# Kernel optimization log

Hardware: AMD Instinct MI355X
Metric: run time of the kernel (lower is better)

## Reference

```python
import jax, jax.numpy as jnp
import numpy as np
from math import pi

BS, H, C = 4096, 1024, 512
H2, C2 = H // 2, C // 2


def _cm(x, y):
    # complex multiply with real/imag stored in last dim
    return jnp.stack([x[..., 0] * y[..., 0] - x[..., 1] * y[..., 1],
                      x[..., 0] * y[..., 1] + x[..., 1] * y[..., 0]], -1)


def _interleave(a, b):
    # (H2, C2),(H2, C2) -> (H, C2) rows [a0,b0,a1,b1,...]
    return jnp.stack([a, b], 1).reshape(-1, a.shape[1])


def _rotations(phi, theta):
    cp, sp = jnp.cos(phi), jnp.sin(phi)
    ct, st = jnp.cos(theta), jnp.sin(theta)
    z = jnp.zeros_like(ct)
    diag = jnp.stack([_interleave(cp * ct, ct), _interleave(sp * ct, z)], -1)      # (H, C2, 2)
    offd = jnp.stack([_interleave(-cp * st, st), _interleave(-sp * st, z)], -1)    # (H, C2, 2)
    return diag.transpose(1, 0, 2), offd.transpose(1, 0, 2)                        # (C2, H, 2)


def _swap_pairs(x):
    # swap elements within adjacent pairs along the hidden axis
    bs, h, _ = x.shape
    return x.reshape(bs, h // 2, 2, 2)[:, :, ::-1, :].reshape(bs, h, 2)


def setup_inputs() -> dict:
    key = jax.random.key(0)
    ks = jax.random.split(key, 5)
    x = jax.random.normal(ks[0], (BS, H, 2), dtype=jnp.float32)
    phi0 = 2 * pi * jax.random.normal(ks[1], (H2, C2), dtype=jnp.float32)
    theta0 = 2 * pi * jax.random.normal(ks[2], (H2, C2), dtype=jnp.float32)
    phi1 = 2 * pi * jax.random.normal(ks[3], (H2, C2), dtype=jnp.float32)
    theta1 = 2 * pi * jax.random.normal(ks[4], (H2, C2), dtype=jnp.float32)
    return {"x": x, "phi0": phi0, "theta0": theta0, "phi1": phi1, "theta1": theta1}


def reference(x, phi0, theta0, phi1, theta1):
    d0, o0 = _rotations(phi0, theta0)
    d1, o1 = _rotations(phi1, theta1)

    def step(xc, dd):
        dd0, oo0, dd1, oo1 = dd
        xc = _cm(xc, dd0) + _cm(_swap_pairs(xc), oo0)
        xc = jnp.roll(xc, -1, axis=1)   # cat(x[1:], x[:1])
        xc = _cm(xc, dd1) + _cm(_swap_pairs(xc), oo1)
        xc = jnp.roll(xc, 1, axis=1)    # cat(x[-1:], x[:-1])
        return xc, None

    x, _ = jax.lax.scan(step, x, (d0, o0, d1, o1))
    return x
```

## Files before the change

### kernel.cpp

```cpp
#include <hip/hip_runtime.h>


#define H_DIM 1024
#define C2 256
#define RPW 2


__global__ __launch_bounds__(256) void eunn_coef_kernel(
    const float* __restrict__ phi0, const float* __restrict__ theta0,
    const float* __restrict__ phi1, const float* __restrict__ theta1,
    float4* __restrict__ coef) {
    int t = blockIdx.x * 256 + threadIdx.x;
    int i = t & 511;
    int p = (t >> 9) & 1;
    int c = t >> 10;
    const float* phi   = p ? phi1   : phi0;
    const float* theta = p ? theta1 : theta0;
    float ph = phi[i * C2 + c];
    float th = theta[i * C2 + c];
    float sp, cp, st, ct;
    __sincosf(ph, &sp, &cp);
    __sincosf(th, &st, &ct);
    int j = i & 7;
    int l = i >> 3;
    coef[(((c * 2 + p) * 8) + j) * 64 + l] = make_float4(ct, st, cp, sp);
}

__device__ __forceinline__ void rot_pair(const float4 q,
                                         float& ur, float& ui,
                                         float& wr, float& wi) {
    float ar = fmaf(-q.y, wr, q.x * ur);
    float ai = fmaf(-q.y, wi, q.x * ui);
    float br = fmaf( q.x, wr, q.y * ur);
    float bi = fmaf( q.x, wi, q.y * ui);
    ur = fmaf(-q.w, ai, q.z * ar);
    ui = fmaf( q.w, ar, q.z * ai);
    wr = br;
    wi = bi;
}

__global__ __launch_bounds__(256, 2) void eunn_main_kernel(
    const float* __restrict__ x,
    const float4* __restrict__ coef,
    float* __restrict__ out) {
    const int lane = threadIdx.x & 63;
    const int wave = threadIdx.x >> 6;
    const int row0 = (blockIdx.x * 4 + wave) * RPW;

    float vr[RPW][16], vi[RPW][16];

#pragma unroll
    for (int r = 0; r < RPW; ++r) {
        const float4* src = (const float4*)(x + (size_t)(row0 + r) * (H_DIM * 2)) + lane * 8;
#pragma unroll
        for (int m = 0; m < 8; ++m) {
            float4 f = src[m];
            vr[r][2 * m]     = f.x; vi[r][2 * m]     = f.y;
            vr[r][2 * m + 1] = f.z; vi[r][2 * m + 1] = f.w;
        }
    }

    const float4* cl = coef + lane;

#pragma unroll 1
    for (int c = 0; c < C2; ++c) {
        const float4* ca = cl + (size_t)c * 1024;

        float4 qq = ca[15 * 64];
        float qpx = __shfl(qq.x, (lane + 63) & 63);
        float qpy = __shfl(qq.y, (lane + 63) & 63);

        {
            float4 q0 = ca[0 * 64];
            float4 q7 = ca[7 * 64];
#pragma unroll
            for (int r = 0; r < RPW; ++r) {
                rot_pair(q0, vr[r][0],  vi[r][0],  vr[r][1],  vi[r][1]);
                rot_pair(q7, vr[r][14], vi[r][14], vr[r][15], vi[r][15]);
            }
        }
        float nbr[RPW], nbi[RPW], pbr[RPW], pbi[RPW];
#pragma unroll
        for (int r = 0; r < RPW; ++r) {
            nbr[r] = __shfl(vr[r][0],  (lane + 1)  & 63);
            nbi[r] = __shfl(vi[r][0],  (lane + 1)  & 63);
            pbr[r] = __shfl(vr[r][15], (lane + 63) & 63);
            pbi[r] = __shfl(vi[r][15], (lane + 63) & 63);
        }

#pragma unroll
        for (int j = 1; j < 7; ++j) {
            float4 q = ca[j * 64];
#pragma unroll
            for (int r = 0; r < RPW; ++r) {
                rot_pair(q, vr[r][2 * j],     vi[r][2 * j],
                            vr[r][2 * j + 1], vi[r][2 * j + 1]);
            }
        }

#pragma unroll
        for (int j = 0; j < 7; ++j) {
            float4 q = ca[(8 + j) * 64];
#pragma unroll
            for (int r = 0; r < RPW; ++r) {
                rot_pair(q, vr[r][2 * j + 1], vi[r][2 * j + 1],
                            vr[r][2 * j + 2], vi[r][2 * j + 2]);
            }
        }

#pragma unroll
        for (int r = 0; r < RPW; ++r) {
            float ar = fmaf(-qq.y, nbr[r], qq.x * vr[r][15]);
            float ai = fmaf(-qq.y, nbi[r], qq.x * vi[r][15]);
            vr[r][15] = fmaf(-qq.w, ai, qq.z * ar);
            vi[r][15] = fmaf( qq.w, ar, qq.z * ai);
            float b0r = fmaf(qpx, vr[r][0], qpy * pbr[r]);
            float b0i = fmaf(qpx, vi[r][0], qpy * pbi[r]);
            vr[r][0] = b0r; vi[r][0] = b0i;
        }
    }

#pragma unroll
    for (int r = 0; r < RPW; ++r) {
        float4* dst = (float4*)(out + (size_t)(row0 + r) * (H_DIM * 2)) + lane * 8;
#pragma unroll
        for (int m = 0; m < 8; ++m) {
            dst[m] = make_float4(vr[r][2 * m],     vi[r][2 * m],
                                 vr[r][2 * m + 1], vi[r][2 * m + 1]);
        }
    }
}

extern "C" void kernel_launch(void* const* d_in, const int* in_sizes, int n_in,
                              void* d_out, int out_size, void* d_ws, size_t ws_size,
                              hipStream_t stream) {
    const float* x      = (const float*)d_in[0];
    const float* phi0   = (const float*)d_in[1];
    const float* theta0 = (const float*)d_in[2];
    const float* phi1   = (const float*)d_in[3];
    const float* theta1 = (const float*)d_in[4];
    float* out = (float*)d_out;
    float4* coef = (float4*)d_ws;

    hipLaunchKernelGGL(eunn_coef_kernel, dim3(1024), dim3(256), 0, stream,
                       phi0, theta0, phi1, theta1, coef);

    hipLaunchKernelGGL(eunn_main_kernel, dim3(512), dim3(256), 0, stream,
                       x, coef, out);
}
```

Baseline: 415.5 us.

## Double-buffer layer coefficients in registers to prefetch next layer during compute

The main loop now preloads the 16 float4 coefficients of the next layer into a second register set while the current layer's rotations run. It unrolls by two to ping-pong between the buffers, and a sched_barrier pins the load placement. The aim is to hide global/L2 load latency on the serial 256-layer chain. The cost is 64 extra VGPRs of coefficient storage, which may pressure the two-blocks-per-CU occupancy, plus one redundant prefetch on the last iteration.

```diff
diff --git a/kernel.cpp b/kernel.cpp
--- a/kernel.cpp
+++ b/kernel.cpp
@@ -46,6 +46,8 @@
     const int lane = threadIdx.x & 63;
     const int wave = threadIdx.x >> 6;
     const int row0 = (blockIdx.x * 4 + wave) * RPW;
+    const int lnext = (lane + 1) & 63;
+    const int lprev = (lane + 63) & 63;
 
     float vr[RPW][16], vi[RPW][16];
 
@@ -62,63 +64,80 @@
 
     const float4* cl = coef + lane;
 
+    float4 A[8], B[8], NA[8], NB[8];
+#pragma unroll
+    for (int j = 0; j < 8; ++j) {
+        A[j] = cl[j * 64];
+        B[j] = cl[(8 + j) * 64];
+    }
+
+#define EUNN_LAYER(A_, B_, NA_, NB_, cnext)                                          \
+    do {                                                                             \
+        const float4* cn_ = cl + (size_t)(cnext) * 1024;                             \
+        float4 qq = B_[7];               \
+        float qpx = __shfl(qq.x, lprev);                        \
+        float qpy = __shfl(qq.y, lprev);                        \
+                               \
+        _Pragma("unroll")                                                            \
+        for (int r = 0; r < RPW; ++r) {                                              \
+            rot_pair(A_[0], vr[r][0],  vi[r][0],  vr[r][1],  vi[r][1]);              \
+            rot_pair(A_[7], vr[r][14], vi[r][14], vr[r][15], vi[r][15]);             \
+        }                                                                            \
+        float nbr[RPW], nbi[RPW], pbr[RPW], pbi[RPW];                                \
+        _Pragma("unroll")                                                            \
+        for (int r = 0; r < RPW; ++r) {                                              \
+            nbr[r] = __shfl(vr[r][0],  lnext);                \
+            nbi[r] = __shfl(vi[r][0],  lnext);                                       \
+            pbr[r] = __shfl(vr[r][15], lprev);               \
+            pbi[r] = __shfl(vi[r][15], lprev);                                       \
+        }                                                                            \
+             \
+        _Pragma("unroll")                                                            \
+        for (int j = 0; j < 8; ++j) { NA_[j] = cn_[j * 64]; }                        \
+        NB_[7] = cn_[15 * 64];                                                       \
+                                                 \
+        _Pragma("unroll")                                                            \
+        for (int j = 1; j < 7; ++j) {                                                \
+            _Pragma("unroll")                                                        \
+            for (int r = 0; r < RPW; ++r)                                            \
+                rot_pair(A_[j], vr[r][2 * j],     vi[r][2 * j],                      \
+                                vr[r][2 * j + 1], vi[r][2 * j + 1]);                 \
+        }                                                                            \
+                                    \
+        _Pragma("unroll")                                                            \
+        for (int j = 0; j < 7; ++j) { NB_[j] = cn_[(8 + j) * 64]; }                  \
+           \
+           \
+        __builtin_amdgcn_sched_barrier(0);                                           \
+                              \
+        _Pragma("unroll")                                                            \
+        for (int j = 0; j < 7; ++j) {                                                \
+            _Pragma("unroll")                                                        \
+            for (int r = 0; r < RPW; ++r)                                            \
+                rot_pair(B_[j], vr[r][2 * j + 1], vi[r][2 * j + 1],                  \
+                                vr[r][2 * j + 2], vi[r][2 * j + 2]);                 \
+        }                                                                            \
+                           \
+        _Pragma("unroll")                                                            \
+        for (int r = 0; r < RPW; ++r) {                                              \
+            float ar = fmaf(-qq.y, nbr[r], qq.x * vr[r][15]);                        \
+            float ai = fmaf(-qq.y, nbi[r], qq.x * vi[r][15]);                        \
+            vr[r][15] = fmaf(-qq.w, ai, qq.z * ar);                                  \
+            vi[r][15] = fmaf( qq.w, ar, qq.z * ai);                                  \
+            float b0r = fmaf(qpx, vr[r][0], qpy * pbr[r]);                           \
+            float b0i = fmaf(qpx, vi[r][0], qpy * pbi[r]);                           \
+            vr[r][0] = b0r; vi[r][0] = b0i;                                          \
+        }                                                                            \
+    } while (0)
+
 #pragma unroll 1
-    for (int c = 0; c < C2; ++c) {
-        const float4* ca = cl + (size_t)c * 1024;
-
-        float4 qq = ca[15 * 64];
-        float qpx = __shfl(qq.x, (lane + 63) & 63);
-        float qpy = __shfl(qq.y, (lane + 63) & 63);
-
-        {
-            float4 q0 = ca[0 * 64];
-            float4 q7 = ca[7 * 64];
-#pragma unroll
-            for (int r = 0; r < RPW; ++r) {
-                rot_pair(q0, vr[r][0],  vi[r][0],  vr[r][1],  vi[r][1]);
-                rot_pair(q7, vr[r][14], vi[r][14], vr[r][15], vi[r][15]);
-            }
-        }
-        float nbr[RPW], nbi[RPW], pbr[RPW], pbi[RPW];
-#pragma unroll
-        for (int r = 0; r < RPW; ++r) {
-            nbr[r] = __shfl(vr[r][0],  (lane + 1)  & 63);
-            nbi[r] = __shfl(vi[r][0],  (lane + 1)  & 63);
-            pbr[r] = __shfl(vr[r][15], (lane + 63) & 63);
-            pbi[r] = __shfl(vi[r][15], (lane + 63) & 63);
-        }
-
-#pragma unroll
-        for (int j = 1; j < 7; ++j) {
-            float4 q = ca[j * 64];
-#pragma unroll
-            for (int r = 0; r < RPW; ++r) {
-                rot_pair(q, vr[r][2 * j],     vi[r][2 * j],
-                            vr[r][2 * j + 1], vi[r][2 * j + 1]);
-            }
-        }
-
-#pragma unroll
-        for (int j = 0; j < 7; ++j) {
-            float4 q = ca[(8 + j) * 64];
-#pragma unroll
-            for (int r = 0; r < RPW; ++r) {
-                rot_pair(q, vr[r][2 * j + 1], vi[r][2 * j + 1],
-                            vr[r][2 * j + 2], vi[r][2 * j + 2]);
-            }
-        }
-
-#pragma unroll
-        for (int r = 0; r < RPW; ++r) {
-            float ar = fmaf(-qq.y, nbr[r], qq.x * vr[r][15]);
-            float ai = fmaf(-qq.y, nbi[r], qq.x * vi[r][15]);
-            vr[r][15] = fmaf(-qq.w, ai, qq.z * ar);
-            vi[r][15] = fmaf( qq.w, ar, qq.z * ai);
-            float b0r = fmaf(qpx, vr[r][0], qpy * pbr[r]);
-            float b0i = fmaf(qpx, vi[r][0], qpy * pbi[r]);
-            vr[r][0] = b0r; vi[r][0] = b0i;
-        }
+    for (int c = 0; c < C2; c += 2) {
+        const int c1  = c + 1;
+        const int c2n = (c + 2 < C2) ? (c + 2) : 0;
+        EUNN_LAYER(A, B, NA, NB, c1);
+        EUNN_LAYER(NA, NB, A, B, c2n);
     }
+#undef EUNN_LAYER
 
 #pragma unroll
     for (int r = 0; r < RPW; ++r) {
```

New measurement: 902.0 us. 117% more time.

## Double-buffer per-step rotation coefficients in LDS via async global_load_lds

Applied to the files above, without the earlier changes.

Each block now stages the 16KB coefficient slab for step c+1 into a shared-memory double buffer with global-to-LDS direct loads while it computes step c, then reads coefficients from LDS. This shares one global fetch among the four waves of a block, where each wave used to fetch the slab itself, and moves load latency off the serial step chain. It adds a block-wide barrier every step and 32KB of LDS per block, which may limit occupancy. The barrier placement relies on the async LDS writes being complete at __syncthreads.

```diff
diff --git a/kernel.cpp b/kernel.cpp
--- a/kernel.cpp
+++ b/kernel.cpp
@@ -46,6 +46,10 @@
     const int lane = threadIdx.x & 63;
     const int wave = threadIdx.x >> 6;
     const int row0 = (blockIdx.x * 4 + wave) * RPW;
+    const int lnext = (lane + 1) & 63;
+    const int lprev = (lane + 63) & 63;
+
+    __shared__ float4 cbuf[2][1024];
 
     float vr[RPW][16], vi[RPW][16];
 
@@ -60,19 +64,36 @@
         }
     }
 
-    const float4* cl = coef + lane;
+#define STAGE(buf_, c_)                                                          \
+    do {                                                                         \
+        const float4* gsrc_ = coef + (size_t)(c_) * 1024 + wave * 256 + lane;    \
+        float4* ldst_ = &cbuf[buf_][wave * 256];                                 \
+        _Pragma("unroll")                                                        \
+        for (int k_ = 0; k_ < 4; ++k_) {                                         \
+            __builtin_amdgcn_global_load_lds(                                    \
+                (const __attribute__((address_space(1))) void*)(gsrc_ + k_ * 64),\
+                (__attribute__((address_space(3))) void*)(ldst_ + k_ * 64),      \
+                16, 0, 0);                                                       \
+        }                                                                        \
+    } while (0)
+
+    STAGE(0, 0);
+    __syncthreads();
 
 #pragma unroll 1
     for (int c = 0; c < C2; ++c) {
-        const float4* ca = cl + (size_t)c * 1024;
+        const int cur = c & 1;
+        if (c + 1 < C2) STAGE(cur ^ 1, c + 1);
 
-        float4 qq = ca[15 * 64];
-        float qpx = __shfl(qq.x, (lane + 63) & 63);
-        float qpy = __shfl(qq.y, (lane + 63) & 63);
+        const float4* cb = &cbuf[cur][lane];
+
+        float4 qq = cb[15 * 64];
+        float qpx = __shfl(qq.x, lprev);
+        float qpy = __shfl(qq.y, lprev);
 
         {
-            float4 q0 = ca[0 * 64];
-            float4 q7 = ca[7 * 64];
+            float4 q0 = cb[0 * 64];
+            float4 q7 = cb[7 * 64];
 #pragma unroll
             for (int r = 0; r < RPW; ++r) {
                 rot_pair(q0, vr[r][0],  vi[r][0],  vr[r][1],  vi[r][1]);
@@ -82,15 +103,15 @@
         float nbr[RPW], nbi[RPW], pbr[RPW], pbi[RPW];
 #pragma unroll
         for (int r = 0; r < RPW; ++r) {
-            nbr[r] = __shfl(vr[r][0],  (lane + 1)  & 63);
-            nbi[r] = __shfl(vi[r][0],  (lane + 1)  & 63);
-            pbr[r] = __shfl(vr[r][15], (lane + 63) & 63);
-            pbi[r] = __shfl(vi[r][15], (lane + 63) & 63);
+            nbr[r] = __shfl(vr[r][0],  lnext);
+            nbi[r] = __shfl(vi[r][0],  lnext);
+            pbr[r] = __shfl(vr[r][15], lprev);
+            pbi[r] = __shfl(vi[r][15], lprev);
         }
 
 #pragma unroll
         for (int j = 1; j < 7; ++j) {
-            float4 q = ca[j * 64];
+            float4 q = cb[j * 64];
 #pragma unroll
             for (int r = 0; r < RPW; ++r) {
                 rot_pair(q, vr[r][2 * j],     vi[r][2 * j],
@@ -100,7 +121,7 @@
 
 #pragma unroll
         for (int j = 0; j < 7; ++j) {
-            float4 q = ca[(8 + j) * 64];
+            float4 q = cb[(8 + j) * 64];
 #pragma unroll
             for (int r = 0; r < RPW; ++r) {
                 rot_pair(q, vr[r][2 * j + 1], vi[r][2 * j + 1],
@@ -118,7 +139,10 @@
             float b0i = fmaf(qpx, vi[r][0], qpy * pbi[r]);
             vr[r][0] = b0r; vi[r][0] = b0i;
         }
+
+        __syncthreads();
     }
+#undef STAGE
 
 #pragma unroll
     for (int r = 0; r < RPW; ++r) {
```

Result: slower. 438.2 us (+5.5%).

## Double-buffer rotation coefficients across layers and process four rows per wave

Applied to the files above, without the earlier changes.

Coefficients for the next layer's first sublayer are prefetched into registers while the current layer's second sublayer runs, and the second-sublayer coefficients are loaded at the top of each iteration. Sched barriers keep these loads issued early so they overlap compute. Rows per wave go from two to four, which halves the grid to 256 blocks and shares each coefficient load across more rows. The cost is much higher register pressure, occupancy dropping to one block per SIMD budget, and only 256 blocks across the GPU, which may underfill the CUs.

```diff
diff --git a/kernel.cpp b/kernel.cpp
--- a/kernel.cpp
+++ b/kernel.cpp
@@ -3,7 +3,7 @@
 
 #define H_DIM 1024
 #define C2 256
-#define RPW 2
+#define RPW 4
 
 
 __global__ __launch_bounds__(256) void eunn_coef_kernel(
@@ -39,13 +39,15 @@
     wi = bi;
 }
 
-__global__ __launch_bounds__(256, 2) void eunn_main_kernel(
+__global__ __launch_bounds__(256, 1) void eunn_main_kernel(
     const float* __restrict__ x,
     const float4* __restrict__ coef,
     float* __restrict__ out) {
     const int lane = threadIdx.x & 63;
     const int wave = threadIdx.x >> 6;
     const int row0 = (blockIdx.x * 4 + wave) * RPW;
+    const int lnext = (lane + 1) & 63;
+    const int lprev = (lane + 63) & 63;
 
     float vr[RPW][16], vi[RPW][16];
 
@@ -62,50 +64,50 @@
 
     const float4* cl = coef + lane;
 
+    float4 A[8], B[8];
+#pragma unroll
+    for (int j = 0; j < 8; ++j) A[j] = cl[j * 64];
+
 #pragma unroll 1
     for (int c = 0; c < C2; ++c) {
-        const float4* ca = cl + (size_t)c * 1024;
+        const float4* cb = cl + (size_t)c * 1024;
 
-        float4 qq = ca[15 * 64];
-        float qpx = __shfl(qq.x, (lane + 63) & 63);
-        float qpy = __shfl(qq.y, (lane + 63) & 63);
+#pragma unroll
+        for (int j = 0; j < 8; ++j) B[j] = cb[(8 + j) * 64];
+        __builtin_amdgcn_sched_barrier(0);
 
-        {
-            float4 q0 = ca[0 * 64];
-            float4 q7 = ca[7 * 64];
 #pragma unroll
-            for (int r = 0; r < RPW; ++r) {
-                rot_pair(q0, vr[r][0],  vi[r][0],  vr[r][1],  vi[r][1]);
-                rot_pair(q7, vr[r][14], vi[r][14], vr[r][15], vi[r][15]);
-            }
+        for (int j = 0; j < 8; ++j) {
+#pragma unroll
+            for (int r = 0; r < RPW; ++r)
+                rot_pair(A[j], vr[r][2 * j],     vi[r][2 * j],
+                               vr[r][2 * j + 1], vi[r][2 * j + 1]);
         }
+
+        float4 qq = B[7];
+        float qpx = __shfl(qq.x, lprev);
+        float qpy = __shfl(qq.y, lprev);
         float nbr[RPW], nbi[RPW], pbr[RPW], pbi[RPW];
 #pragma unroll
         for (int r = 0; r < RPW; ++r) {
-            nbr[r] = __shfl(vr[r][0],  (lane + 1)  & 63);
-            nbi[r] = __shfl(vi[r][0],  (lane + 1)  & 63);
-            pbr[r] = __shfl(vr[r][15], (lane + 63) & 63);
-            pbi[r] = __shfl(vi[r][15], (lane + 63) & 63);
+            nbr[r] = __shfl(vr[r][0],  lnext);
+            nbi[r] = __shfl(vi[r][0],  lnext);
+            pbr[r] = __shfl(vr[r][15], lprev);
+            pbi[r] = __shfl(vi[r][15], lprev);
         }
 
+        const int cn = (c + 1 < C2) ? (c + 1) : 0;
+        const float4* cnp = cl + (size_t)cn * 1024;
 #pragma unroll
-        for (int j = 1; j < 7; ++j) {
-            float4 q = ca[j * 64];
-#pragma unroll
-            for (int r = 0; r < RPW; ++r) {
-                rot_pair(q, vr[r][2 * j],     vi[r][2 * j],
-                            vr[r][2 * j + 1], vi[r][2 * j + 1]);
-            }
-        }
+        for (int j = 0; j < 8; ++j) A[j] = cnp[j * 64];
+        __builtin_amdgcn_sched_barrier(0);
 
 #pragma unroll
         for (int j = 0; j < 7; ++j) {
-            float4 q = ca[(8 + j) * 64];
 #pragma unroll
-            for (int r = 0; r < RPW; ++r) {
-                rot_pair(q, vr[r][2 * j + 1], vi[r][2 * j + 1],
-                            vr[r][2 * j + 2], vi[r][2 * j + 2]);
-            }
+            for (int r = 0; r < RPW; ++r)
+                rot_pair(B[j], vr[r][2 * j + 1], vi[r][2 * j + 1],
+                               vr[r][2 * j + 2], vi[r][2 * j + 2]);
         }
 
 #pragma unroll
@@ -145,6 +147,6 @@
     hipLaunchKernelGGL(eunn_coef_kernel, dim3(1024), dim3(256), 0, stream,
                        phi0, theta0, phi1, theta1, coef);
 
-    hipLaunchKernelGGL(eunn_main_kernel, dim3(512), dim3(256), 0, stream,
+    hipLaunchKernelGGL(eunn_main_kernel, dim3(256), dim3(256), 0, stream,
                        x, coef, out);
 }
```

After: 457.5 us. +10.1%, slower.
